# Kernel optimization log

Hardware: AMD Instinct MI355X
Metric: run time of the kernel (lower is better)

## Reference

```python
import jax, jax.numpy as jnp
import numpy as np

N_NODES = 100000
N_EDGES = 600000
IN_SIZE = 128
NUM_HEADS = 8
OUT_DIM = 16  # out_size // num_heads = 128 // 8
NEG_SLOPE = 0.2


def setup_inputs() -> dict:
    key = jax.random.key(0)
    k1, k2, k3, k4, k5, k6, k7 = jax.random.split(key, 7)
    h = jax.random.normal(k1, (N_NODES, IN_SIZE), dtype=jnp.float32)
    o = jax.random.normal(k2, (N_NODES, NUM_HEADS * OUT_DIM), dtype=jnp.float32)
    # scale params for numerical sanity of exp() in edge softmax
    W = jax.random.normal(k3, (IN_SIZE, NUM_HEADS * OUT_DIM), dtype=jnp.float32) * 0.05
    attn_l = jax.random.normal(k4, (NUM_HEADS, OUT_DIM), dtype=jnp.float32) * 0.05
    attn_r = jax.random.normal(k5, (NUM_HEADS, OUT_DIM), dtype=jnp.float32) * 0.05
    src = jax.random.randint(k6, (N_EDGES,), 0, N_NODES, dtype=jnp.int64)
    dst = jax.random.randint(k7, (N_EDGES,), 0, N_NODES, dtype=jnp.int64)
    return {"h": h, "o": o, "W": W, "attn_l": attn_l, "attn_r": attn_r,
            "src": src, "dst": dst}


def reference(h, o, W, attn_l, attn_r, src, dst):
    N = h.shape[0]
    # linear projection -> per-head features [N, H, D]
    z = (h @ W).reshape(N, NUM_HEADS, OUT_DIM)
    # per-node attention logit halves [N, H]
    el = jnp.einsum('nhd,hd->nh', z, attn_l)
    er = jnp.einsum('nhd,hd->nh', z, attn_r)
    # per-edge score: message src -> dst, LeakyReLU  [E, H]
    e = jax.nn.leaky_relu(el[dst] + er[src], negative_slope=NEG_SLOPE)
    # edge softmax over incoming edges of each destination node
    m = jax.ops.segment_max(e, dst, num_segments=N)          # [N, H]
    ex = jnp.exp(e - m[dst])                                  # [E, H]
    s = jax.ops.segment_sum(ex, dst, num_segments=N)          # [N, H]
    alpha = ex / s[dst]                                       # [E, H]
    # weighted aggregate of source features  [N, H, D]
    msg = alpha[:, :, None] * z[src]                          # [E, H, D]
    agg = jax.ops.segment_sum(msg, dst, num_segments=N)
    # merge='cat' -> [N, H*D]; residual + ELU
    out = agg.reshape(N, NUM_HEADS * OUT_DIM)
    return o + jax.nn.elu(out)
```

## Files before the change

kernel.cpp:

```cpp
#include <hip/hip_runtime.h>
#include <hip/hip_bf16.h>
#include <math.h>

#define NNODES 100000
#define NEDGES 600000
#define IN 128
#define HD 128
#define NH 8
#define NEG_SLOPE 0.2f
#define RG_TOTAL (NNODES / 16)
#define NFRAG 36
#define CT_ALL 9
#define NPAD 100352
#define SCAN_BLOCKS 98
#define PACK_BLOCKS 9
#define HIST4_BLOCKS ((NEDGES / 4 + 255) / 256)
#define GEMM_BLOCKS 782

typedef __attribute__((ext_vector_type(8))) short short8v;
typedef __attribute__((ext_vector_type(4))) float f32x4;

__device__ inline unsigned short f2bf(float f) {
    unsigned u = __float_as_uint(f);
    unsigned r = (u + 0x7fff + ((u >> 16) & 1)) >> 16;
    return (unsigned short)r;
}
__device__ inline float bflo(unsigned v) { return __uint_as_float(v << 16); }
__device__ inline float bfhi(unsigned v) { return __uint_as_float(v & 0xffff0000u); }
__device__ inline unsigned cvtpk(float lo, float hi) {
    unsigned r;
    asm("v_cvt_pk_bf16_f32 %0, %1, %2" : "=v"(r) : "v"(lo), "v"(hi));
    return r;
}

__global__ __launch_bounds__(256) void k_pack_hist(
    const float* __restrict__ W, const float* __restrict__ attn_l, const float* __restrict__ attn_r,
    short8v* __restrict__ Wb,
    const int* __restrict__ dst, int* __restrict__ cnt, int* __restrict__ rank)
{
    const int tid = threadIdx.x;
    if (blockIdx.x < PACK_BLOCKS) {
        int slot = blockIdx.x * 256 + tid;
        int f = slot >> 6, lane = slot & 63;
        int ks = f / CT_ALL, ct = f % CT_ALL;
        int k0 = ks * 32 + (lane >> 4) * 8;
        short8v v;
        if (ct < 8) {
            int col = ct * 16 + (lane & 15);
            #pragma unroll
            for (int j = 0; j < 8; ++j) v[j] = (short)f2bf(W[(k0 + j) * HD + col]);
        } else {
            int c = lane & 15;
            const float* av = (c < 8) ? attn_l : attn_r;
            int hh = c & 7;
            #pragma unroll
            for (int j = 0; j < 8; ++j) {
                int k = k0 + j;
                float s = 0.f;
                for (int d = 0; d < 16; ++d) s += W[k * HD + hh * 16 + d] * av[hh * 16 + d];
                v[j] = (short)f2bf(s);
            }
        }
        Wb[slot] = v;
    } else {
        int e0 = ((blockIdx.x - PACK_BLOCKS) * 256 + tid) * 4;
        if (e0 < NEDGES) {
            int4 d4 = *(const int4*)(dst + e0);
            int4 r4;
            r4.x = atomicAdd(&cnt[d4.x], 1);
            r4.y = atomicAdd(&cnt[d4.y], 1);
            r4.z = atomicAdd(&cnt[d4.z], 1);
            r4.w = atomicAdd(&cnt[d4.w], 1);
            *(int4*)(rank + e0) = r4;
        }
    }
}

__global__ __launch_bounds__(256) void k_gemm_scan1(
    const float* __restrict__ h, const short8v* __restrict__ Wb,
    unsigned short* __restrict__ z, float* __restrict__ el, float* __restrict__ er,
    const int* __restrict__ cnt, int* __restrict__ inc, int* __restrict__ bsum)
{
    __shared__ short8v Bs[NFRAG * 64];
    __shared__ int sd[2][256];
    const int tid = threadIdx.x;

    if (blockIdx.x < SCAN_BLOCKS) {
        int gid4 = blockIdx.x * 256 + tid;
        int4 v = ((const int4*)cnt)[gid4];
        int s1 = v.x + v.y, s2 = s1 + v.z, s3 = s2 + v.w;
        sd[0][tid] = s3; __syncthreads();
        int cur = 0;
        for (int off = 1; off < 256; off <<= 1) {
            int nv = sd[cur][tid] + (tid >= off ? sd[cur][tid - off] : 0);
            sd[cur ^ 1][tid] = nv; __syncthreads();
            cur ^= 1;
        }
        int incl = sd[cur][tid];
        int eb = incl - s3;
        int4 w = make_int4(eb + v.x, eb + s1, eb + s2, eb + s3);
        ((int4*)inc)[gid4] = w;
        if (tid == 255) bsum[blockIdx.x] = incl;
        return;
    }

    {
        const float4* srcp = (const float4*)Wb;
        float4* dstp = (float4*)Bs;
        for (int i = tid; i < NFRAG * 64; i += 256) dstp[i] = srcp[i];
    }
    __syncthreads();

    const int lane  = tid & 63;
    const int rowIn = lane & 15;
    const int kgrp  = lane >> 4;
    int wid = ((blockIdx.x - SCAN_BLOCKS) * 256 + tid) >> 6;
    const int nw = GEMM_BLOCKS * 4;

    for (int rg = wid; rg < RG_TOTAL; rg += nw) {
        const int row0 = rg * 16;
        const float* hp = h + (size_t)(row0 + rowIn) * IN + kgrp * 8;

        short8v afr[4];
        #pragma unroll
        for (int ks = 0; ks < 4; ++ks) {
            float4 a0 = *(const float4*)(hp + ks * 32);
            float4 a1 = *(const float4*)(hp + ks * 32 + 4);
            uint4 u;
            u.x = cvtpk(a0.x, a0.y);
            u.y = cvtpk(a0.z, a0.w);
            u.z = cvtpk(a1.x, a1.y);
            u.w = cvtpk(a1.z, a1.w);
            afr[ks] = __builtin_bit_cast(short8v, u);
        }

        f32x4 acc[CT_ALL];
        #pragma unroll
        for (int ct = 0; ct < CT_ALL; ++ct) acc[ct] = (f32x4){0.f, 0.f, 0.f, 0.f};

        #pragma unroll
        for (int ks = 0; ks < 4; ++ks)
            #pragma unroll
            for (int ct = 0; ct < CT_ALL; ++ct)
                acc[ct] = __builtin_amdgcn_mfma_f32_16x16x32_bf16(
                    Bs[(ks * CT_ALL + ct) * 64 + lane], afr[ks], acc[ct], 0, 0, 0);

        const size_t zrow = (size_t)(row0 + rowIn) * HD;
        #pragma unroll
        for (int ct = 0; ct < 8; ++ct) {
            uint2 pk;
            pk.x = cvtpk(acc[ct][0], acc[ct][1]);
            pk.y = cvtpk(acc[ct][2], acc[ct][3]);
            *(uint2*)(z + zrow + ct * 16 + kgrp * 4) = pk;
        }
        {
            float4 v = make_float4(acc[8][0], acc[8][1], acc[8][2], acc[8][3]);
            int row = row0 + rowIn;
            if (kgrp < 2) *(float4*)(el + row * NH + kgrp * 4) = v;
            else          *(float4*)(er + row * NH + (kgrp - 2) * 4) = v;
        }
    }
}

__global__ __launch_bounds__(256) void kscan23(
    const int* __restrict__ cnt, const int* __restrict__ inc, const int* __restrict__ bsum,
    int* __restrict__ offs)
{
    __shared__ int bs[2][128];
    const int tid = threadIdx.x;
    if (tid < 128) bs[0][tid] = (tid < SCAN_BLOCKS) ? bsum[tid] : 0;
    __syncthreads();
    int cur = 0;
    for (int off = 1; off < 128; off <<= 1) {
        if (tid < 128) {
            int nv = bs[cur][tid] + (tid >= off ? bs[cur][tid - off] : 0);
            bs[cur ^ 1][tid] = nv;
        }
        __syncthreads();
        cur ^= 1;
    }
    const int base = (blockIdx.x == 0) ? 0 : bs[cur][blockIdx.x - 1];

    int gid4 = blockIdx.x * 256 + tid;
    int4 c = ((const int4*)cnt)[gid4];
    int4 ic = ((const int4*)inc)[gid4];
    int i0 = gid4 * 4;
    int ex[4] = { base + ic.x - c.x, base + ic.y - c.y, base + ic.z - c.z, base + ic.w - c.w };
    #pragma unroll
    for (int j = 0; j < 4; ++j) {
        int i = i0 + j;
        if (i < NNODES) offs[i] = ex[j];
        else if (i == NNODES) offs[i] = NEDGES;
    }
}

__global__ void k_scatter(const int* __restrict__ src, const int* __restrict__ dst,
                          const int* __restrict__ rank, const int* __restrict__ offs,
                          int* __restrict__ esrc) {
    int e0 = (blockIdx.x * blockDim.x + threadIdx.x) * 4;
    if (e0 >= NEDGES) return;
    int4 s4 = *(const int4*)(src + e0);
    int4 d4 = *(const int4*)(dst + e0);
    int4 r4 = *(const int4*)(rank + e0);
    esrc[offs[d4.x] + r4.x] = s4.x;
    esrc[offs[d4.y] + r4.y] = s4.y;
    esrc[offs[d4.z] + r4.z] = s4.z;
    esrc[offs[d4.w] + r4.w] = s4.w;
}

__global__ __launch_bounds__(256) void k_agg(
    const int* __restrict__ offs, const int* __restrict__ esrc,
    const float* __restrict__ el, const float* __restrict__ er,
    const unsigned short* __restrict__ z, const float* __restrict__ o,
    float* __restrict__ out)
{
    const int wid  = (blockIdx.x * blockDim.x + threadIdx.x) >> 6;
    const int lane = threadIdx.x & 63;
    if (wid >= NNODES) return;
    const int d  = wid;
    const int p0 = offs[d];
    const int n  = offs[d + 1] - p0;
    const int g  = lane & 31;
    const int e2 = lane >> 5;
    const int hh = g >> 2;
    const float el8 = el[d * NH + hh];

    const size_t obase = (size_t)d * HD + g * 4;
    const f32x4 ov = __builtin_nontemporal_load((const f32x4*)(o + obase));

    float srun = 0.f;
    f32x4 acc = (f32x4){0.f, 0.f, 0.f, 0.f};

    for (int c0 = 0; c0 < n; c0 += 64) {
        const int m = (n - c0 < 64) ? (n - c0) : 64;
        int sid = __builtin_nontemporal_load(esrc + p0 + c0 + (lane < m ? lane : 0));

        for (int b = 0; b < m; b += 8) {
            float erv[4]; uint2 zb[4];
            #pragma unroll
            for (int k = 0; k < 4; ++k) {
                int ei = b + k * 2 + e2;
                int eic = (ei < m) ? ei : 0;
                int s = __shfl(sid, eic, 64);
                erv[k] = er[s * NH + hh];
                zb[k]  = *(const uint2*)(z + (size_t)s * HD + g * 4);
            }
            #pragma unroll
            for (int k = 0; k < 4; ++k) {
                int ei = b + k * 2 + e2;
                float ev = el8 + erv[k];
                ev = fmaxf(ev, NEG_SLOPE * ev);
                float ex = (ei < m) ? __expf(ev) : 0.f;
                srun += ex;
                acc[0] = fmaf(ex, bflo(zb[k].x), acc[0]);
                acc[1] = fmaf(ex, bfhi(zb[k].x), acc[1]);
                acc[2] = fmaf(ex, bflo(zb[k].y), acc[2]);
                acc[3] = fmaf(ex, bfhi(zb[k].y), acc[3]);
            }
        }
    }

    srun   += __shfl_xor(srun, 32, 64);
    acc[0] += __shfl_xor(acc[0], 32, 64);
    acc[1] += __shfl_xor(acc[1], 32, 64);
    acc[2] += __shfl_xor(acc[2], 32, 64);
    acc[3] += __shfl_xor(acc[3], 32, 64);

    if (lane < 32) {
        float inv = (srun > 0.f) ? 1.f / srun : 0.f;
        float r0 = acc[0] * inv, r1 = acc[1] * inv, r2 = acc[2] * inv, r3 = acc[3] * inv;
        r0 = (r0 > 0.f) ? r0 : expm1f(r0);
        r1 = (r1 > 0.f) ? r1 : expm1f(r1);
        r2 = (r2 > 0.f) ? r2 : expm1f(r2);
        r3 = (r3 > 0.f) ? r3 : expm1f(r3);
        f32x4 res = (f32x4){ov[0] + r0, ov[1] + r1, ov[2] + r2, ov[3] + r3};
        __builtin_nontemporal_store(res, (f32x4*)(out + obase));
    }
}

extern "C" void kernel_launch(void* const* d_in, const int* in_sizes, int n_in,
                              void* d_out, int out_size, void* d_ws, size_t ws_size,
                              hipStream_t stream) {
    const float* h      = (const float*)d_in[0];
    const float* o      = (const float*)d_in[1];
    const float* W      = (const float*)d_in[2];
    const float* attn_l = (const float*)d_in[3];
    const float* attn_r = (const float*)d_in[4];
    const int*   src    = (const int*)d_in[5];
    const int*   dst    = (const int*)d_in[6];
    float* out = (float*)d_out;

    char* ws = (char*)d_ws;
    unsigned short* z = (unsigned short*)(ws);
    float* el     = (float*)(ws + 25600000);
    float* er     = (float*)(ws + 28800000);
    int*   cnt    = (int*)  (ws + 32000000);
    int*   inc    = (int*)  (ws + 32401408);
    int*   offs   = (int*)  (ws + 32802816);
    int*   rank   = (int*)  (ws + 33202832);
    int*   bsum   = (int*)  (ws + 35602832);
    int*   esrc   = (int*)  (ws + 35603344);
    short8v* Wb   = (short8v*)(ws + 38003344);

    hipMemsetAsync(cnt, 0, NPAD * sizeof(int), stream);

    k_pack_hist<<<PACK_BLOCKS + HIST4_BLOCKS, 256, 0, stream>>>(W, attn_l, attn_r, Wb, dst, cnt, rank);
    k_gemm_scan1<<<SCAN_BLOCKS + GEMM_BLOCKS, 256, 0, stream>>>(h, Wb, z, el, er, cnt, inc, bsum);
    kscan23<<<SCAN_BLOCKS, 256, 0, stream>>>(cnt, inc, bsum, offs);
    k_scatter<<<(NEDGES / 4 + 255) / 256, 256, 0, stream>>>(src, dst, rank, offs, esrc);
    k_agg<<<(NNODES * 64 + 255) / 256, 256, 0, stream>>>(offs, esrc, el, er, z, o, out);
}
```

Baseline: 121.4 us.

## Restructure CSR build pipeline: fold block-scan into scatter, overlap scatter with GEMM

Splits the per-block count scan into its own small kernel, then merges the global block-offset scan and the edge scatter into the GEMM launch, so the scatter runs alongside the projection GEMM. The offs array is dropped: both scatter and aggregation rebuild offsets from block bases plus per-block exclusive prefixes, and degree comes from cnt. It also folds log2(e) into the packed attention weights so the aggregation can call exp2 directly instead of exp. The net effect is one fewer launch and a less serialized scan/scatter chain. In exchange, every scatter block re-runs the 128-entry scan, and el/er are now stored scaled by log2(e).

```diff
diff --git a/kernel.cpp b/kernel.cpp
--- a/kernel.cpp
+++ b/kernel.cpp
@@ -8,6 +8,7 @@
 #define HD 128
 #define NH 8
 #define NEG_SLOPE 0.2f
+#define LOG2E 1.44269504f
 #define RG_TOTAL (NNODES / 16)
 #define NFRAG 36
 #define CT_ALL 9
@@ -15,6 +16,7 @@
 #define SCAN_BLOCKS 98
 #define PACK_BLOCKS 9
 #define HIST4_BLOCKS ((NEDGES / 4 + 255) / 256)
+#define SCATTER_BLOCKS HIST4_BLOCKS
 #define GEMM_BLOCKS 782
 
 typedef __attribute__((ext_vector_type(8))) short short8v;
@@ -58,7 +60,7 @@
                 int k = k0 + j;
                 float s = 0.f;
                 for (int d = 0; d < 16; ++d) s += W[k * HD + hh * 16 + d] * av[hh * 16 + d];
-                v[j] = (short)f2bf(s);
+                v[j] = (short)f2bf(s * LOG2E);
             }
         }
         Wb[slot] = v;
@@ -76,31 +78,67 @@
     }
 }
 
-__global__ __launch_bounds__(256) void k_gemm_scan1(
+__global__ __launch_bounds__(256) void k_scan1(
+    const int* __restrict__ cnt, int* __restrict__ excl, int* __restrict__ bsum)
+{
+    __shared__ int sd[2][256];
+    const int tid = threadIdx.x;
+    int gid4 = blockIdx.x * 256 + tid;
+    int4 v = ((const int4*)cnt)[gid4];
+    int s1 = v.x + v.y, s2 = s1 + v.z, s3 = s2 + v.w;
+    sd[0][tid] = s3; __syncthreads();
+    int cur = 0;
+    for (int off = 1; off < 256; off <<= 1) {
+        int nv = sd[cur][tid] + (tid >= off ? sd[cur][tid - off] : 0);
+        sd[cur ^ 1][tid] = nv; __syncthreads();
+        cur ^= 1;
+    }
+    int incl = sd[cur][tid];
+    int eb = incl - s3;
+    ((int4*)excl)[gid4] = make_int4(eb, eb + v.x, eb + s1, eb + s2);
+    if (tid == 255) bsum[blockIdx.x] = incl;
+}
+
+__global__ __launch_bounds__(256) void k_scatter_gemm(
+    const int* __restrict__ src, const int* __restrict__ dst, const int* __restrict__ rank,
+    const int* __restrict__ excl, const int* __restrict__ bsum,
+    int* __restrict__ esrc, int* __restrict__ bbase,
     const float* __restrict__ h, const short8v* __restrict__ Wb,
-    unsigned short* __restrict__ z, float* __restrict__ el, float* __restrict__ er,
-    const int* __restrict__ cnt, int* __restrict__ inc, int* __restrict__ bsum)
+    unsigned short* __restrict__ z, float* __restrict__ el, float* __restrict__ er)
 {
     __shared__ short8v Bs[NFRAG * 64];
-    __shared__ int sd[2][256];
+    __shared__ int bs[2][128];
     const int tid = threadIdx.x;
 
-    if (blockIdx.x < SCAN_BLOCKS) {
-        int gid4 = blockIdx.x * 256 + tid;
-        int4 v = ((const int4*)cnt)[gid4];
-        int s1 = v.x + v.y, s2 = s1 + v.z, s3 = s2 + v.w;
-        sd[0][tid] = s3; __syncthreads();
+    if (blockIdx.x < SCATTER_BLOCKS) {
+        if (tid < 128) bs[0][tid] = (tid < SCAN_BLOCKS) ? bsum[tid] : 0;
+        __syncthreads();
         int cur = 0;
-        for (int off = 1; off < 256; off <<= 1) {
-            int nv = sd[cur][tid] + (tid >= off ? sd[cur][tid - off] : 0);
-            sd[cur ^ 1][tid] = nv; __syncthreads();
+        for (int off = 1; off < 128; off <<= 1) {
+            if (tid < 128) {
+                int nv = bs[cur][tid] + (tid >= off ? bs[cur][tid - off] : 0);
+                bs[cur ^ 1][tid] = nv;
+            }
+            __syncthreads();
             cur ^= 1;
         }
-        int incl = sd[cur][tid];
-        int eb = incl - s3;
-        int4 w = make_int4(eb + v.x, eb + s1, eb + s2, eb + s3);
-        ((int4*)inc)[gid4] = w;
-        if (tid == 255) bsum[blockIdx.x] = incl;
+        if (blockIdx.x == 0 && tid < 128)
+            bbase[tid] = (tid == 0) ? 0 : bs[cur][tid - 1];
+
+        int e0 = (blockIdx.x * 256 + tid) * 4;
+        if (e0 < NEDGES) {
+            int4 s4 = *(const int4*)(src + e0);
+            int4 d4 = *(const int4*)(dst + e0);
+            int4 r4 = *(const int4*)(rank + e0);
+            int b0 = (d4.x >> 10) ? bs[cur][(d4.x >> 10) - 1] : 0;
+            int b1 = (d4.y >> 10) ? bs[cur][(d4.y >> 10) - 1] : 0;
+            int b2 = (d4.z >> 10) ? bs[cur][(d4.z >> 10) - 1] : 0;
+            int b3 = (d4.w >> 10) ? bs[cur][(d4.w >> 10) - 1] : 0;
+            esrc[b0 + excl[d4.x] + r4.x] = s4.x;
+            esrc[b1 + excl[d4.y] + r4.y] = s4.y;
+            esrc[b2 + excl[d4.z] + r4.z] = s4.z;
+            esrc[b3 + excl[d4.w] + r4.w] = s4.w;
+        }
         return;
     }
 
@@ -114,7 +152,7 @@
     const int lane  = tid & 63;
     const int rowIn = lane & 15;
     const int kgrp  = lane >> 4;
-    int wid = ((blockIdx.x - SCAN_BLOCKS) * 256 + tid) >> 6;
+    int wid = ((blockIdx.x - SCATTER_BLOCKS) * 256 + tid) >> 6;
     const int nw = GEMM_BLOCKS * 4;
 
     for (int rg = wid; rg < RG_TOTAL; rg += nw) {
@@ -162,54 +200,9 @@
     }
 }
 
-__global__ __launch_bounds__(256) void kscan23(
-    const int* __restrict__ cnt, const int* __restrict__ inc, const int* __restrict__ bsum,
-    int* __restrict__ offs)
-{
-    __shared__ int bs[2][128];
-    const int tid = threadIdx.x;
-    if (tid < 128) bs[0][tid] = (tid < SCAN_BLOCKS) ? bsum[tid] : 0;
-    __syncthreads();
-    int cur = 0;
-    for (int off = 1; off < 128; off <<= 1) {
-        if (tid < 128) {
-            int nv = bs[cur][tid] + (tid >= off ? bs[cur][tid - off] : 0);
-            bs[cur ^ 1][tid] = nv;
-        }
-        __syncthreads();
-        cur ^= 1;
-    }
-    const int base = (blockIdx.x == 0) ? 0 : bs[cur][blockIdx.x - 1];
-
-    int gid4 = blockIdx.x * 256 + tid;
-    int4 c = ((const int4*)cnt)[gid4];
-    int4 ic = ((const int4*)inc)[gid4];
-    int i0 = gid4 * 4;
-    int ex[4] = { base + ic.x - c.x, base + ic.y - c.y, base + ic.z - c.z, base + ic.w - c.w };
-    #pragma unroll
-    for (int j = 0; j < 4; ++j) {
-        int i = i0 + j;
-        if (i < NNODES) offs[i] = ex[j];
-        else if (i == NNODES) offs[i] = NEDGES;
-    }
-}
-
-__global__ void k_scatter(const int* __restrict__ src, const int* __restrict__ dst,
-                          const int* __restrict__ rank, const int* __restrict__ offs,
-                          int* __restrict__ esrc) {
-    int e0 = (blockIdx.x * blockDim.x + threadIdx.x) * 4;
-    if (e0 >= NEDGES) return;
-    int4 s4 = *(const int4*)(src + e0);
-    int4 d4 = *(const int4*)(dst + e0);
-    int4 r4 = *(const int4*)(rank + e0);
-    esrc[offs[d4.x] + r4.x] = s4.x;
-    esrc[offs[d4.y] + r4.y] = s4.y;
-    esrc[offs[d4.z] + r4.z] = s4.z;
-    esrc[offs[d4.w] + r4.w] = s4.w;
-}
-
 __global__ __launch_bounds__(256) void k_agg(
-    const int* __restrict__ offs, const int* __restrict__ esrc,
+    const int* __restrict__ excl, const int* __restrict__ cnt, const int* __restrict__ bbase,
+    const int* __restrict__ esrc,
     const float* __restrict__ el, const float* __restrict__ er,
     const unsigned short* __restrict__ z, const float* __restrict__ o,
     float* __restrict__ out)
@@ -218,8 +211,8 @@
     const int lane = threadIdx.x & 63;
     if (wid >= NNODES) return;
     const int d  = wid;
-    const int p0 = offs[d];
-    const int n  = offs[d + 1] - p0;
+    const int p0 = bbase[d >> 10] + excl[d];
+    const int n  = cnt[d];
     const int g  = lane & 31;
     const int e2 = lane >> 5;
     const int hh = g >> 2;
@@ -250,7 +243,7 @@
                 int ei = b + k * 2 + e2;
                 float ev = el8 + erv[k];
                 ev = fmaxf(ev, NEG_SLOPE * ev);
-                float ex = (ei < m) ? __expf(ev) : 0.f;
+                float ex = (ei < m) ? __builtin_exp2f(ev) : 0.f;
                 srun += ex;
                 acc[0] = fmaf(ex, bflo(zb[k].x), acc[0]);
                 acc[1] = fmaf(ex, bfhi(zb[k].x), acc[1]);
@@ -295,18 +288,18 @@
     float* el     = (float*)(ws + 25600000);
     float* er     = (float*)(ws + 28800000);
     int*   cnt    = (int*)  (ws + 32000000);
-    int*   inc    = (int*)  (ws + 32401408);
-    int*   offs   = (int*)  (ws + 32802816);
-    int*   rank   = (int*)  (ws + 33202832);
-    int*   bsum   = (int*)  (ws + 35602832);
-    int*   esrc   = (int*)  (ws + 35603344);
-    short8v* Wb   = (short8v*)(ws + 38003344);
+    int*   excl   = (int*)  (ws + 32401408);
+    int*   rank   = (int*)  (ws + 32802816);
+    int*   bsum   = (int*)  (ws + 35202816);
+    int*   bbase  = (int*)  (ws + 35203328);
+    int*   esrc   = (int*)  (ws + 35203840);
+    short8v* Wb   = (short8v*)(ws + 37603840);
 
     hipMemsetAsync(cnt, 0, NPAD * sizeof(int), stream);
 
     k_pack_hist<<<PACK_BLOCKS + HIST4_BLOCKS, 256, 0, stream>>>(W, attn_l, attn_r, Wb, dst, cnt, rank);
-    k_gemm_scan1<<<SCAN_BLOCKS + GEMM_BLOCKS, 256, 0, stream>>>(h, Wb, z, el, er, cnt, inc, bsum);
-    kscan23<<<SCAN_BLOCKS, 256, 0, stream>>>(cnt, inc, bsum, offs);
-    k_scatter<<<(NEDGES / 4 + 255) / 256, 256, 0, stream>>>(src, dst, rank, offs, esrc);
-    k_agg<<<(NNODES * 64 + 255) / 256, 256, 0, stream>>>(offs, esrc, el, er, z, o, out);
-}
+    k_scan1<<<SCAN_BLOCKS, 256, 0, stream>>>(cnt, excl, bsum);
+    k_scatter_gemm<<<SCATTER_BLOCKS + GEMM_BLOCKS, 256, 0, stream>>>(
+        src, dst, rank, excl, bsum, esrc, bbase, h, Wb, z, el, er);
+    k_agg<<<(NNODES * 64 + 255) / 256, 256, 0, stream>>>(excl, cnt, bbase, esrc, el, er, z, o, out);
+}
```

New measurement: 122.3 us. Within noise of the previous version (+0.7%).
